# Kernel tuning notes

Measured on AMD Instinct MI355X. Metric: run time of the kernel, lower is better.

The kernel has to match this reference:

```python
import jax, jax.numpy as jnp
import numpy as np

B, CIN, COUT, K, H, W = 16, 128, 256, 3, 56, 56
STRIDE = 1
PAD = K // 2


def setup_inputs() -> dict:
    key = jax.random.key(0)
    ks = jax.random.split(key, 12)
    x = jax.random.normal(ks[0], (B, CIN, H, W), dtype=jnp.float32)
    base_kernel = jax.random.normal(ks[1], (COUT, CIN, K, K), dtype=jnp.float32)
    bias = jnp.zeros((COUT,), dtype=jnp.float32)
    s = 1.0 / np.sqrt(CIN)
    fc_spatial_w = jax.random.uniform(ks[2], (K * K, CIN), minval=-s, maxval=s)
    fc_spatial_b = jax.random.uniform(ks[3], (K * K,), minval=-s, maxval=s)
    fc_in_w = jax.random.uniform(ks[4], (CIN, CIN), minval=-s, maxval=s)
    fc_in_b = jax.random.uniform(ks[5], (CIN,), minval=-s, maxval=s)
    fc_out_w = jax.random.uniform(ks[6], (COUT, CIN), minval=-s, maxval=s)
    fc_out_b = jax.random.uniform(ks[7], (COUT,), minval=-s, maxval=s)
    fc_kernel_w = jax.random.uniform(ks[8], (COUT * CIN * K * K, CIN), minval=-s, maxval=s)
    fc_kernel_b = jax.random.uniform(ks[9], (COUT * CIN * K * K,), minval=-s, maxval=s)
    return {
        "x": x, "base_kernel": base_kernel, "bias": bias,
        "fc_spatial_w": fc_spatial_w, "fc_spatial_b": fc_spatial_b,
        "fc_in_w": fc_in_w, "fc_in_b": fc_in_b,
        "fc_out_w": fc_out_w, "fc_out_b": fc_out_b,
        "fc_kernel_w": fc_kernel_w, "fc_kernel_b": fc_kernel_b,
    }


def _odconv(x, base_kernel, bias, fc_spatial_w, fc_spatial_b, fc_in_w, fc_in_b,
            fc_out_w, fc_out_b, fc_kernel_w, fc_kernel_b):
    b = x.shape[0]
    # global average pool -> context [B, Cin]
    context = jnp.mean(x, axis=(2, 3))
    sig = jax.nn.sigmoid
    attn_spatial = sig(context @ fc_spatial_w.T + fc_spatial_b).reshape(b, 1, 1, K, K)
    attn_in = sig(context @ fc_in_w.T + fc_in_b).reshape(b, 1, CIN, 1, 1)
    attn_out = sig(context @ fc_out_w.T + fc_out_b).reshape(b, COUT, 1, 1, 1)
    attn_kernel = sig(context @ fc_kernel_w.T + fc_kernel_b).reshape(b, COUT, CIN, K, K)
    # 5-way broadcast multiply -> per-sample dynamic kernel [B, Cout, Cin, K, K]
    dyn = base_kernel[None] * attn_out * attn_in * attn_spatial * attn_kernel

    def conv_one(xi, wi):
        # xi: [Cin, H, W], wi: [Cout, Cin, K, K]
        out = jax.lax.conv_general_dilated(
            xi[None], wi,
            window_strides=(STRIDE, STRIDE),
            padding=[(PAD, PAD), (PAD, PAD)],
            dimension_numbers=("NCHW", "OIHW", "NCHW"),
        )
        return out[0]

    out = jax.vmap(conv_one)(x, dyn)  # [B, Cout, H', W']
    return out + bias[None, :, None, None]


def reference(x, base_kernel, bias, fc_spatial_w, fc_spatial_b, fc_in_w, fc_in_b,
              fc_out_w, fc_out_b, fc_kernel_w, fc_kernel_b):
    return _odconv(x, base_kernel, bias, fc_spatial_w, fc_spatial_b, fc_in_w, fc_in_b,
                   fc_out_w, fc_out_b, fc_kernel_w, fc_kernel_b)
```

## Files before the change

### kernel.cpp

```cpp
#include <hip/hip_runtime.h>
#include <hip/hip_bf16.h>
#include <math.h>

#define BATCH 16
#define CIN   128
#define COUT  256
#define HH    56
#define WW    56
#define HW    3136
#define NTAP  9
#define NE    (COUT*CIN*NTAP)

typedef short short8 __attribute__((ext_vector_type(8)));
typedef float floatx4 __attribute__((ext_vector_type(4)));

#define WSB_CTX   0
#define WSB_ASP   8192
#define WSB_AIN   9472
#define WSB_AOUT  17664
#define WSB_XT    34048
#define WSB_DYN   (WSB_XT + BATCH*HW*CIN*2)

static __device__ inline unsigned short f2b(float f) {
    union { float f; unsigned u; } v; v.f = f;
    unsigned r = v.u + 0x7FFF + ((v.u >> 16) & 1);
    return (unsigned short)(r >> 16);
}
static __device__ inline short8 pack8(float4 a, float4 b) {
    short8 r;
    r[0] = (short)f2b(a.x); r[1] = (short)f2b(a.y); r[2] = (short)f2b(a.z); r[3] = (short)f2b(a.w);
    r[4] = (short)f2b(b.x); r[5] = (short)f2b(b.y); r[6] = (short)f2b(b.z); r[7] = (short)f2b(b.w);
    return r;
}

__global__ void k_context(const float* __restrict__ x, float* __restrict__ ctx) {
    int bc = blockIdx.x;
    const float4* p = (const float4*)(x + (size_t)bc * HW);
    float s = 0.f;
    for (int i = threadIdx.x; i < HW / 4; i += 256) { float4 v = p[i]; s += v.x + v.y + v.z + v.w; }
    for (int off = 32; off; off >>= 1) s += __shfl_down(s, off, 64);
    __shared__ float red[4];
    if ((threadIdx.x & 63) == 0) red[threadIdx.x >> 6] = s;
    __syncthreads();
    if (threadIdx.x == 0) ctx[bc] = (red[0] + red[1] + red[2] + red[3]) * (1.f / (float)HW);
}

__global__ void k_xt(const float* __restrict__ x, unsigned short* __restrict__ xt) {
    int b = blockIdx.y;
    int p = blockIdx.x * 64 + (threadIdx.x & 63);
    int icq = threadIdx.x >> 6;
    const float* xb = x + (size_t)b * CIN * HW + p;
    unsigned short tmp[32];
#pragma unroll
    for (int j = 0; j < 32; ++j) tmp[j] = f2b(xb[(size_t)(icq * 32 + j) * HW]);
    uint4* dst = (uint4*)(xt + ((size_t)b * HW + p) * CIN + icq * 32);
    const uint4* s = (const uint4*)tmp;
    dst[0] = s[0]; dst[1] = s[1]; dst[2] = s[2]; dst[3] = s[3];
}

__global__ void k_attn(const float* __restrict__ ctx,
                       const float* __restrict__ wsp, const float* __restrict__ bsp,
                       const float* __restrict__ win, const float* __restrict__ bin,
                       const float* __restrict__ wout, const float* __restrict__ bout,
                       float* __restrict__ asp, float* __restrict__ ain, float* __restrict__ aout) {
    int R = blockIdx.x * 4 + (threadIdx.x >> 6);
    int lane = threadIdx.x & 63;
    int b = R / 393, r = R % 393;
    const float* w; float bias; float* o;
    if (r < 9)        { w = wsp  + r * CIN;         bias = bsp[r];         o = asp  + b * 16  + r; }
    else if (r < 137) { w = win  + (r - 9) * CIN;   bias = bin[r - 9];     o = ain  + b * CIN + (r - 9); }
    else              { w = wout + (r - 137) * CIN; bias = bout[r - 137];  o = aout + b * COUT + (r - 137); }
    float2 wv = ((const float2*)w)[lane];
    float2 cv = ((const float2*)(ctx + b * CIN))[lane];
    float d = wv.x * cv.x + wv.y * cv.y;
    for (int off = 32; off; off >>= 1) d += __shfl_down(d, off, 64);
    if (lane == 0) *o = 1.f / (1.f + __expf(-(d + bias)));
}

__global__ void k_build(const float* __restrict__ ctx, const float* __restrict__ wk,
                        const float* __restrict__ bk, const float* __restrict__ base,
                        const float* __restrict__ asp, const float* __restrict__ ain,
                        const float* __restrict__ aout, unsigned short* __restrict__ dyn) {
    int wid = threadIdx.x >> 6, l = threadIdx.x & 63;
    int lq = l & 15, quad = l >> 4;
    short8 afr[4];
    const float* arow = ctx + lq * CIN;
#pragma unroll
    for (int kc = 0; kc < 4; ++kc) {
        float4 v0 = *(const float4*)(arow + kc * 32 + quad * 8);
        float4 v1 = *(const float4*)(arow + kc * 32 + quad * 8 + 4);
        afr[kc] = pack8(v0, v1);
    }
    int n0w = blockIdx.x * 256 + wid * 64;
    for (int nf = 0; nf < 4; ++nf) {
        int n0 = n0w + nf * 16;
        int ic  = (n0 & 127) + lq;
        int oc  = (n0 >> 7) & 255;
        int tap = n0 >> 15;
        int e = (oc * CIN + ic) * NTAP + tap;
        const float* wrow = wk + (size_t)e * CIN;
        floatx4 acc = {0.f, 0.f, 0.f, 0.f};
#pragma unroll
        for (int kc = 0; kc < 4; ++kc) {
            float4 v0 = *(const float4*)(wrow + kc * 32 + quad * 8);
            float4 v1 = *(const float4*)(wrow + kc * 32 + quad * 8 + 4);
            short8 bfr = pack8(v0, v1);
            acc = __builtin_amdgcn_mfma_f32_16x16x32_bf16(afr[kc], bfr, acc, 0, 0, 0);
        }
        float bke = bk[e], bse = base[e];
#pragma unroll
        for (int r = 0; r < 4; ++r) {
            int b = quad * 4 + r;
            float s = 1.f / (1.f + __expf(-(acc[r] + bke)));
            float v = bse * s * aout[b * COUT + oc] * ain[b * CIN + ic] * asp[b * 16 + tap];
            dyn[(size_t)b * NE + n0 + lq] = f2b(v);
        }
    }
}

__global__ __launch_bounds__(256, 2) void k_conv(
    const unsigned short* __restrict__ xt, const unsigned short* __restrict__ dyn,
    const float* __restrict__ bias, float* __restrict__ out) {
    __shared__ char s_x[580 * 64];
    __shared__ char s_a[576 * 64];
    int b = blockIdx.z, oc0 = blockIdx.y * 64, r0 = blockIdx.x * 8;
    int tid = threadIdx.x;
    int wn = tid >> 6, l = tid & 63, lq = l & 15, quad = l >> 4;
    const unsigned short* xtb  = xt  + (size_t)b * HW * CIN;
    const unsigned short* dynb = dyn + (size_t)b * NE;

    int pixaddr[7];
#pragma unroll
    for (int nf = 0; nf < 7; ++nf) {
        int n = nf * 16 + lq;
        int tr = wn * 2 + n / 56, col = n % 56;
        pixaddr[nf] = (tr * 58 + col) * 64 + quad * 16;
    }

    floatx4 acc[4][7];
#pragma unroll
    for (int i = 0; i < 4; ++i)
#pragma unroll
        for (int j = 0; j < 7; ++j) acc[i][j] = (floatx4){0.f, 0.f, 0.f, 0.f};

    for (int kc = 0; kc < 4; ++kc) {
        __syncthreads();
        for (int u = tid; u < 2320; u += 256) {
            int icq = u & 3, pix = u >> 2;
            int ry = pix / 58, cx = pix % 58;
            int gy = r0 + ry - 1, gx = cx - 1;
            uint4 v = {0u, 0u, 0u, 0u};
            if (gy >= 0 && gy < HH && gx >= 0 && gx < WW)
                v = *(const uint4*)(xtb + (size_t)(gy * WW + gx) * CIN + kc * 32 + icq * 8);
            *(uint4*)(s_x + pix * 64 + icq * 16) = v;
        }
        for (int u = tid; u < 2304; u += 256) {
            int icq = u & 3, oc = (u >> 2) & 63, tap = u >> 8;
            *(uint4*)(s_a + u * 16) =
                *(const uint4*)(dynb + (size_t)(tap * COUT + oc0 + oc) * CIN + kc * 32 + icq * 8);
        }
        __syncthreads();
#pragma unroll
        for (int tap = 0; tap < 9; ++tap) {
            short8 af[4];
#pragma unroll
            for (int mf = 0; mf < 4; ++mf)
                af[mf] = *(const short8*)(s_a + (tap * 64 + mf * 16 + lq) * 64 + quad * 16);
            int toff = ((tap / 3) * 58 + (tap % 3)) * 64;
#pragma unroll
            for (int nf = 0; nf < 7; ++nf) {
                short8 bf = *(const short8*)(s_x + pixaddr[nf] + toff);
#pragma unroll
                for (int mf = 0; mf < 4; ++mf)
                    acc[mf][nf] = __builtin_amdgcn_mfma_f32_16x16x32_bf16(af[mf], bf, acc[mf][nf], 0, 0, 0);
            }
        }
    }

#pragma unroll
    for (int mf = 0; mf < 4; ++mf) {
#pragma unroll
        for (int r = 0; r < 4; ++r) {
            int oc = oc0 + mf * 16 + quad * 4 + r;
            float bs = bias[oc];
            float* ob = out + (size_t)(b * COUT + oc) * HW + (r0 + wn * 2) * 56 + lq;
#pragma unroll
            for (int nf = 0; nf < 7; ++nf)
                ob[nf * 16] = acc[mf][nf][r] + bs;
        }
    }
}

extern "C" void kernel_launch(void* const* d_in, const int* in_sizes, int n_in,
                              void* d_out, int out_size, void* d_ws, size_t ws_size,
                              hipStream_t stream) {
    const float* x    = (const float*)d_in[0];
    const float* base = (const float*)d_in[1];
    const float* bias = (const float*)d_in[2];
    const float* wsp  = (const float*)d_in[3];
    const float* bsp  = (const float*)d_in[4];
    const float* win  = (const float*)d_in[5];
    const float* bin  = (const float*)d_in[6];
    const float* wout = (const float*)d_in[7];
    const float* bout = (const float*)d_in[8];
    const float* wk   = (const float*)d_in[9];
    const float* bk   = (const float*)d_in[10];
    float* out = (float*)d_out;
    char* ws = (char*)d_ws;

    float* ctx  = (float*)(ws + WSB_CTX);
    float* asp  = (float*)(ws + WSB_ASP);
    float* ain  = (float*)(ws + WSB_AIN);
    float* aout = (float*)(ws + WSB_AOUT);
    unsigned short* xt  = (unsigned short*)(ws + WSB_XT);
    unsigned short* dyn = (unsigned short*)(ws + WSB_DYN);

    k_context<<<BATCH * CIN, 256, 0, stream>>>(x, ctx);
    k_xt<<<dim3(HW / 64, BATCH), 256, 0, stream>>>(x, xt);
    k_attn<<<(BATCH * 393) / 4, 256, 0, stream>>>(ctx, wsp, bsp, win, bin, wout, bout, asp, ain, aout);
    k_build<<<NE / 256, 256, 0, stream>>>(ctx, wk, bk, base, asp, ain, aout, dyn);
    k_conv<<<dim3(HH / 8, COUT / 64, BATCH), 256, 0, stream>>>(xt, dyn, bias, out);
}
```

Before: 332.5 us.

## Fuse transpose into dynamic-kernel build launch and remap conv block order

Merges the x-transpose kernel into the dynamic-kernel build kernel as extra blocks of one launch, so the two independent jobs share the GPU and one launch is dropped. The conv grid is flattened to 1D with a swizzled block-to-(batch, oc tile, row tile) mapping, intended to group blocks that share the same input rows or weights for better cache reuse. The halo load loop is restructured so each thread handles a fixed column and channel quarter across 10 rows, removing the per-element divide and modulo. The fused kernel's register and launch footprint is now sized for the heavier build path, which may lower occupancy for the transpose blocks.

```diff
diff --git a/kernel.cpp b/kernel.cpp
--- a/kernel.cpp
+++ b/kernel.cpp
@@ -43,19 +43,6 @@
     if ((threadIdx.x & 63) == 0) red[threadIdx.x >> 6] = s;
     __syncthreads();
     if (threadIdx.x == 0) ctx[bc] = (red[0] + red[1] + red[2] + red[3]) * (1.f / (float)HW);
-}
-
-__global__ void k_xt(const float* __restrict__ x, unsigned short* __restrict__ xt) {
-    int b = blockIdx.y;
-    int p = blockIdx.x * 64 + (threadIdx.x & 63);
-    int icq = threadIdx.x >> 6;
-    const float* xb = x + (size_t)b * CIN * HW + p;
-    unsigned short tmp[32];
-#pragma unroll
-    for (int j = 0; j < 32; ++j) tmp[j] = f2b(xb[(size_t)(icq * 32 + j) * HW]);
-    uint4* dst = (uint4*)(xt + ((size_t)b * HW + p) * CIN + icq * 32);
-    const uint4* s = (const uint4*)tmp;
-    dst[0] = s[0]; dst[1] = s[1]; dst[2] = s[2]; dst[3] = s[3];
 }
 
 __global__ void k_attn(const float* __restrict__ ctx,
@@ -77,10 +64,28 @@
     if (lane == 0) *o = 1.f / (1.f + __expf(-(d + bias)));
 }
 
-__global__ void k_build(const float* __restrict__ ctx, const float* __restrict__ wk,
-                        const float* __restrict__ bk, const float* __restrict__ base,
-                        const float* __restrict__ asp, const float* __restrict__ ain,
-                        const float* __restrict__ aout, unsigned short* __restrict__ dyn) {
+#define XT_BLOCKS    784
+#define BUILD_BLOCKS 1152
+__global__ void k_fat(const float* __restrict__ x, unsigned short* __restrict__ xt,
+                      const float* __restrict__ ctx, const float* __restrict__ wk,
+                      const float* __restrict__ bk, const float* __restrict__ base,
+                      const float* __restrict__ asp, const float* __restrict__ ain,
+                      const float* __restrict__ aout, unsigned short* __restrict__ dyn) {
+    if (blockIdx.x < XT_BLOCKS) {
+        int bid = blockIdx.x;
+        int b = bid / 49;
+        int p = (bid % 49) * 64 + (threadIdx.x & 63);
+        int icq = threadIdx.x >> 6;
+        const float* xb = x + (size_t)b * CIN * HW + p;
+        unsigned short tmp[32];
+#pragma unroll
+        for (int j = 0; j < 32; ++j) tmp[j] = f2b(xb[(size_t)(icq * 32 + j) * HW]);
+        uint4* dst = (uint4*)(xt + ((size_t)b * HW + p) * CIN + icq * 32);
+        const uint4* s = (const uint4*)tmp;
+        dst[0] = s[0]; dst[1] = s[1]; dst[2] = s[2]; dst[3] = s[3];
+        return;
+    }
+    int bid = blockIdx.x - XT_BLOCKS;
     int wid = threadIdx.x >> 6, l = threadIdx.x & 63;
     int lq = l & 15, quad = l >> 4;
     short8 afr[4];
@@ -91,7 +96,7 @@
         float4 v1 = *(const float4*)(arow + kc * 32 + quad * 8 + 4);
         afr[kc] = pack8(v0, v1);
     }
-    int n0w = blockIdx.x * 256 + wid * 64;
+    int n0w = bid * 256 + wid * 64;
     for (int nf = 0; nf < 4; ++nf) {
         int n0 = n0w + nf * 16;
         int ic  = (n0 & 127) + lq;
@@ -123,7 +128,16 @@
     const float* __restrict__ bias, float* __restrict__ out) {
     __shared__ char s_x[580 * 64];
     __shared__ char s_a[576 * 64];
-    int b = blockIdx.z, oc0 = blockIdx.y * 64, r0 = blockIdx.x * 8;
+    int id  = blockIdx.x;
+    int low = id & 7;
+    int q   = id >> 3;
+    int r   = q % 7;
+    int phi = q / 7;
+    int p   = phi * 8 + low;
+    int oc0 = (p >> 4) * 64;
+    int b   = p & 15;
+    int r0  = r * 8;
+
     int tid = threadIdx.x;
     int wn = tid >> 6, l = tid & 63, lq = l & 15, quad = l >> 4;
     const unsigned short* xtb  = xt  + (size_t)b * HW * CIN;
@@ -143,21 +157,24 @@
 #pragma unroll
         for (int j = 0; j < 7; ++j) acc[i][j] = (floatx4){0.f, 0.f, 0.f, 0.f};
 
+    int cx  = tid & 63;
+    int icq = tid >> 6;
     for (int kc = 0; kc < 4; ++kc) {
         __syncthreads();
-        for (int u = tid; u < 2320; u += 256) {
-            int icq = u & 3, pix = u >> 2;
-            int ry = pix / 58, cx = pix % 58;
-            int gy = r0 + ry - 1, gx = cx - 1;
-            uint4 v = {0u, 0u, 0u, 0u};
-            if (gy >= 0 && gy < HH && gx >= 0 && gx < WW)
-                v = *(const uint4*)(xtb + (size_t)(gy * WW + gx) * CIN + kc * 32 + icq * 8);
-            *(uint4*)(s_x + pix * 64 + icq * 16) = v;
+#pragma unroll
+        for (int ry = 0; ry < 10; ++ry) {
+            if (cx < 58) {
+                int gy = r0 + ry - 1, gx = cx - 1;
+                uint4 v = {0u, 0u, 0u, 0u};
+                if (gy >= 0 && gy < HH && gx >= 0 && gx < WW)
+                    v = *(const uint4*)(xtb + (size_t)(gy * WW + gx) * CIN + kc * 32 + icq * 8);
+                *(uint4*)(s_x + (ry * 58 + cx) * 64 + icq * 16) = v;
+            }
         }
         for (int u = tid; u < 2304; u += 256) {
-            int icq = u & 3, oc = (u >> 2) & 63, tap = u >> 8;
+            int icq2 = u & 3, oc = (u >> 2) & 63, tap = u >> 8;
             *(uint4*)(s_a + u * 16) =
-                *(const uint4*)(dynb + (size_t)(tap * COUT + oc0 + oc) * CIN + kc * 32 + icq * 8);
+                *(const uint4*)(dynb + (size_t)(tap * COUT + oc0 + oc) * CIN + kc * 32 + icq2 * 8);
         }
         __syncthreads();
 #pragma unroll
@@ -180,13 +197,13 @@
 #pragma unroll
     for (int mf = 0; mf < 4; ++mf) {
 #pragma unroll
-        for (int r = 0; r < 4; ++r) {
-            int oc = oc0 + mf * 16 + quad * 4 + r;
+        for (int rr = 0; rr < 4; ++rr) {
+            int oc = oc0 + mf * 16 + quad * 4 + rr;
             float bs = bias[oc];
             float* ob = out + (size_t)(b * COUT + oc) * HW + (r0 + wn * 2) * 56 + lq;
 #pragma unroll
             for (int nf = 0; nf < 7; ++nf)
-                ob[nf * 16] = acc[mf][nf][r] + bs;
+                ob[nf * 16] = acc[mf][nf][rr] + bs;
         }
     }
 }
@@ -216,8 +233,7 @@
     unsigned short* dyn = (unsigned short*)(ws + WSB_DYN);
 
     k_context<<<BATCH * CIN, 256, 0, stream>>>(x, ctx);
-    k_xt<<<dim3(HW / 64, BATCH), 256, 0, stream>>>(x, xt);
     k_attn<<<(BATCH * 393) / 4, 256, 0, stream>>>(ctx, wsp, bsp, win, bin, wout, bout, asp, ain, aout);
-    k_build<<<NE / 256, 256, 0, stream>>>(ctx, wk, bk, base, asp, ain, aout, dyn);
-    k_conv<<<dim3(HH / 8, COUT / 64, BATCH), 256, 0, stream>>>(xt, dyn, bias, out);
-}
+    k_fat<<<XT_BLOCKS + BUILD_BLOCKS, 256, 0, stream>>>(x, xt, ctx, wk, bk, base, asp, ain, aout, dyn);
+    k_conv<<<448, 256, 0, stream>>>(xt, dyn, bias, out);
+}
```

Measured after the change: 322.4 us. 3.0% less time.
